# Optimization experiments

Measured on AMD Instinct MI355X. Metric: run time of the kernel, lower is better.

The kernel has to match this reference:

```python
import jax, jax.numpy as jnp
import numpy as np

N, E, G = 50000, 800000, 128
F_IN, H, NHID, C = 310, 128, 64, 2  # H = 2*nhid
NEG_SLOPE = 0.2


def setup_inputs() -> dict:
    key = jax.random.key(0)
    ks = jax.random.split(key, 16)
    def lin(k, fan_in, shape):
        return (jax.random.normal(k, shape, jnp.float32) / np.sqrt(fan_in)).astype(jnp.float32)
    return {
        "x": jax.random.normal(ks[0], (N, F_IN), jnp.float32),
        "edge_index": jax.random.randint(ks[1], (2, E), 0, N, dtype=jnp.int32),
        "batch": jnp.sort(jax.random.randint(ks[2], (N,), 0, G, dtype=jnp.int32)),
        "W1": lin(ks[3], F_IN, (F_IN, H)),
        "a_src1": lin(ks[4], H, (H,)),
        "a_dst1": lin(ks[5], H, (H,)),
        "b1": jnp.zeros((H,), jnp.float32),
        "W2": lin(ks[6], H, (H, H)),
        "a_src2": lin(ks[7], H, (H,)),
        "a_dst2": lin(ks[8], H, (H,)),
        "b2": jnp.zeros((H,), jnp.float32),
        "fc1_w": lin(ks[9], H, (H, NHID)),
        "fc1_b": jnp.zeros((NHID,), jnp.float32),
        "fc2_w": lin(ks[10], NHID, (NHID, C)),
        "fc2_b": jnp.zeros((C,), jnp.float32),
    }


def _gat(x, src, dst, W, a_src, a_dst, b):
    # PyG GATConv, heads=1: h = xW; e_ij = LeakyReLU(a_src.h_j + a_dst.h_i)
    h = x @ W                               # [N, H]
    asrc = h @ a_src                        # [N]
    adst = h @ a_dst                        # [N]
    e = jax.nn.leaky_relu(asrc[src] + adst[dst], NEG_SLOPE)  # [E']
    # segment softmax over incoming edges of each target node
    m = jax.ops.segment_max(e, dst, num_segments=N)
    ex = jnp.exp(e - m[dst])
    s = jax.ops.segment_sum(ex, dst, num_segments=N)
    w = ex / s[dst]                         # [E']
    out = jax.ops.segment_sum(h[src] * w[:, None], dst, num_segments=N)
    return out + b


def reference(x, edge_index, batch, W1, a_src1, a_dst1, b1,
              W2, a_src2, a_dst2, b2, fc1_w, fc1_b, fc2_w, fc2_b):
    # add self loops (GATConv default add_self_loops=True)
    ar = jnp.arange(N, dtype=edge_index.dtype)
    src = jnp.concatenate([edge_index[0], ar])
    dst = jnp.concatenate([edge_index[1], ar])

    h = jax.nn.selu(_gat(x, src, dst, W1, a_src1, a_dst1, b1))
    h = jax.nn.selu(_gat(h, src, dst, W2, a_src2, a_dst2, b2))

    # global mean pool over graphs
    summed = jax.ops.segment_sum(h, batch, num_segments=G)          # [G, H]
    cnt = jax.ops.segment_sum(jnp.ones((N,), h.dtype), batch, num_segments=G)
    pooled = jax.nn.selu(summed / jnp.maximum(cnt, 1.0)[:, None])

    z = jax.nn.selu(pooled @ fc1_w + fc1_b)  # dropout is identity in eval
    logits = z @ fc2_w + fc2_b
    return jax.nn.log_softmax(logits, axis=-1)
```

## Files before the change

### kernel.cpp

```cpp
#include <hip/hip_runtime.h>
#include <hip/hip_bf16.h>
#include <math.h>

#define NN 50000
#define NE 800000
#define NET (NE + NN)
#define FIN 310
#define HD 128
#define NHID 64
#define NCLS 2
#define NG 128
#define NEG_SLOPE 0.2f
#define KP1 320
#define KP2 128

#define SLOTS 64
#define NPART 8
#define PART_SZ (NN / NPART)
#define EPB 4096
#define NSLICE ((NET + EPB - 1) / EPB)
#define NSC (NSLICE * NPART)
#define GB1 ((NN + 63) / 64)
#define CASTW_GRID ((NE + 255) / 256)

#define SELU_SCALE 1.0507009873554804934193349852946f
#define SELU_ALPHA 1.6732632423543772848170429916717f

typedef short bf16x8 __attribute__((ext_vector_type(8)));
typedef float f32x4 __attribute__((ext_vector_type(4)));

__device__ __forceinline__ float selu(float x) {
    return SELU_SCALE * (x > 0.f ? x : SELU_ALPHA * (__expf(x) - 1.f));
}
__device__ __forceinline__ float lrelu(float x) {
    return x > 0.f ? x : NEG_SLOPE * x;
}
__device__ __forceinline__ unsigned short f2bf(float f) {
    unsigned int u = __float_as_uint(f);
    u = (u + 0x7fffu + ((u >> 16) & 1u)) >> 16;
    return (unsigned short)u;
}
__device__ __forceinline__ float bf2f(unsigned short b) {
    return __uint_as_float(((unsigned int)b) << 16);
}


__global__ void k_castW(const float* __restrict__ W1, const float* __restrict__ W2,
                        const int* __restrict__ ei,
                        unsigned short* __restrict__ W1p, unsigned short* __restrict__ W2p,
                        unsigned int* __restrict__ ep, int* __restrict__ cursor) {
    int i = blockIdx.x * blockDim.x + threadIdx.x;
    if (i < NN) cursor[i] = 0;
    const int N1 = HD * KP1;
    if (i < N1) {
        int n = i / KP1, k = i % KP1;
        unsigned short v = (k < FIN) ? f2bf(W1[(size_t)k * HD + n]) : (unsigned short)0;
        W1p[((k >> 3) * HD + n) * 8 + (k & 7)] = v;
    } else if (i - N1 < HD * KP2) {
        int j = i - N1;
        int n = j / KP2, k = j % KP2;
        W2p[((k >> 3) * HD + n) * 8 + (k & 7)] = f2bf(W2[(size_t)k * HD + n]);
    }
    if (i < NE)
        ep[i] = ((unsigned int)ei[i] << 16) | (unsigned int)ei[NE + i];
}


__device__ __forceinline__ void scatter_body(int slice, const unsigned int* __restrict__ ep,
                                             int* __restrict__ cursor,
                                             unsigned short* __restrict__ slots,
                                             int part) {
    int lo = part * PART_SZ;
    int base = slice * EPB + threadIdx.x;
#pragma unroll
    for (int k = 0; k < EPB / 256; ++k) {
        int i = base + k * 256;
        if (i >= NET) break;
        int d, s;
        if (i < NE) {
            unsigned int e = ep[i];
            d = (int)(e & 0xffffu);
            s = (int)(e >> 16);
        } else {
            d = i - NE; s = d;
        }
        if ((unsigned)(d - lo) < (unsigned)PART_SZ) {
            int pos = atomicAdd(&cursor[d], 1) & (SLOTS - 1);
            slots[(size_t)d * SLOTS + pos] = (unsigned short)s;
        }
    }
}


#define RGEMM_EPILOGUE                                                         \
    int gr_base = r0 + w * 16 + quad * 4;                                      \
    _Pragma("unroll")                                                          \
    for (int r = 0; r < 4; ++r) {                                              \
        int gr = gr_base + r;                                                  \
        if (gr < M) {                                                          \
            _Pragma("unroll")                                                  \
            for (int nt = 0; nt < 8; ++nt)                                     \
                C[(size_t)gr * HD + nt * 16 + l16] = f2bf(acc[nt][r]);         \
        }                                                                      \
    }                                                                          \
    _Pragma("unroll")                                                          \
    for (int r = 0; r < 4; ++r) {                                              \
        float s1 = 0.f, s2 = 0.f;                                              \
        _Pragma("unroll")                                                      \
        for (int nt = 0; nt < 8; ++nt) {                                       \
            int c = nt * 16 + l16;                                             \
            float v = acc[nt][r];                                              \
            s1 += v * a_src[c];                                                \
            s2 += v * a_dst[c];                                                \
        }                                                                      \
        _Pragma("unroll")                                                      \
        for (int off = 1; off < 16; off <<= 1) {                               \
            s1 += __shfl_xor(s1, off);                                         \
            s2 += __shfl_xor(s2, off);                                         \
        }                                                                      \
        int gr = gr_base + r;                                                  \
        if (l16 == 0 && gr < M) { asrcp[gr] = s1; adstp[gr] = s2; }            \
    }


__global__ __launch_bounds__(256) void k_pre(const float* __restrict__ A,
                                             const unsigned short* __restrict__ Bp,
                                             unsigned short* __restrict__ C,
                                             float* __restrict__ asrcp,
                                             float* __restrict__ adstp,
                                             const float* __restrict__ a_src,
                                             const float* __restrict__ a_dst,
                                             int M,
                                             const unsigned int* __restrict__ ep,
                                             int* __restrict__ cursor,
                                             unsigned short* __restrict__ slots) {
    if (blockIdx.x >= GB1) {
        int b = blockIdx.x - GB1;
        int part = (blockIdx.x + 2) & 7;
        scatter_body(b >> 3, ep, cursor, slots, part);
        return;
    }
    int t = threadIdx.x;
    int lane = t & 63, w = t >> 6;
    int quad = lane >> 4, l16 = lane & 15;
    int r0 = blockIdx.x * 64;

    int grow = r0 + w * 16 + l16;
    int arow = min(grow, M - 1);
    const float* ap = A + (size_t)arow * FIN + quad * 8;

    f32x4 acc[8] = {};

    float2 c0 = *(const float2*)(ap + 0);
    float2 c1 = *(const float2*)(ap + 2);
    float2 c2 = *(const float2*)(ap + 4);
    float2 c3 = *(const float2*)(ap + 6);
#pragma unroll
    for (int k0 = 0; k0 < 288; k0 += 32) {
        int kn = (k0 < 256) ? k0 + 32 : 256;
        float2 n0 = *(const float2*)(ap + kn + 0);
        float2 n1 = *(const float2*)(ap + kn + 2);
        float2 n2 = *(const float2*)(ap + kn + 4);
        float2 n3 = *(const float2*)(ap + kn + 6);
        union { bf16x8 v; unsigned short u[8]; } af;
        af.u[0] = f2bf(c0.x); af.u[1] = f2bf(c0.y);
        af.u[2] = f2bf(c1.x); af.u[3] = f2bf(c1.y);
        af.u[4] = f2bf(c2.x); af.u[5] = f2bf(c2.y);
        af.u[6] = f2bf(c3.x); af.u[7] = f2bf(c3.y);
        const unsigned short* bbase = Bp + ((size_t)(k0 >> 3) + quad) * (HD * 8) + l16 * 8;
#pragma unroll
        for (int nt = 0; nt < 8; ++nt) {
            bf16x8 bfr = *(const bf16x8*)(bbase + nt * 128);
            acc[nt] = __builtin_amdgcn_mfma_f32_16x16x32_bf16(af.v, bfr, acc[nt], 0, 0, 0);
        }
        c0 = n0; c1 = n1; c2 = n2; c3 = n3;
    }
    {
        int kb = 288 + quad * 8;
        const float* rp = A + (size_t)arow * FIN;
        union { bf16x8 v; unsigned short u[8]; } af;
#pragma unroll
        for (int j = 0; j < 8; ++j)
            af.u[j] = (kb + j < FIN) ? f2bf(rp[kb + j]) : (unsigned short)0;
        const unsigned short* bbase = Bp + ((size_t)(288 >> 3) + quad) * (HD * 8) + l16 * 8;
#pragma unroll
        for (int nt = 0; nt < 8; ++nt) {
            bf16x8 bfr = *(const bf16x8*)(bbase + nt * 128);
            acc[nt] = __builtin_amdgcn_mfma_f32_16x16x32_bf16(af.v, bfr, acc[nt], 0, 0, 0);
        }
    }
    RGEMM_EPILOGUE
}


__global__ __launch_bounds__(256) void k_gemm2(const unsigned short* __restrict__ A,
                                               const unsigned short* __restrict__ Bp,
                                               unsigned short* __restrict__ C,
                                               float* __restrict__ asrcp,
                                               float* __restrict__ adstp,
                                               const float* __restrict__ a_src,
                                               const float* __restrict__ a_dst,
                                               int M) {
    int t = threadIdx.x;
    int lane = t & 63, w = t >> 6;
    int quad = lane >> 4, l16 = lane & 15;
    int r0 = blockIdx.x * 64;

    int grow = r0 + w * 16 + l16;
    int arow = min(grow, M - 1);
    const unsigned short* aptr = A + (size_t)arow * KP2 + quad * 8;

    f32x4 acc[8] = {};
#pragma unroll
    for (int k0 = 0; k0 < KP2; k0 += 32) {
        bf16x8 af = *(const bf16x8*)(aptr + k0);
        const unsigned short* bbase = Bp + ((size_t)(k0 >> 3) + quad) * (HD * 8) + l16 * 8;
#pragma unroll
        for (int nt = 0; nt < 8; ++nt) {
            bf16x8 bfr = *(const bf16x8*)(bbase + nt * 128);
            acc[nt] = __builtin_amdgcn_mfma_f32_16x16x32_bf16(af, bfr, acc[nt], 0, 0, 0);
        }
    }
    RGEMM_EPILOGUE
}


__global__ __launch_bounds__(256) void k_gat(const unsigned short* __restrict__ h,
                                             const float* __restrict__ asrc,
                                             const float* __restrict__ adst,
                                             const int* __restrict__ degv,
                                             const unsigned short* __restrict__ slots,
                                             const float* __restrict__ bias,
                                             unsigned short* __restrict__ out) {
    int node = blockIdx.x * 4 + (threadIdx.x >> 6);
    int lane = threadIdx.x & 63;
    if (node >= NN) return;
    int g = lane >> 4, cl = lane & 15;
    int deg = degv[node];
    float adsti = adst[node];

    float2 acc2[4] = {};

    int cnt = min(deg, SLOTS);
    int s_c = 0; float p_c = 0.f;
    if (lane < cnt) {
        s_c = slots[(size_t)node * SLOTS + lane];
        p_c = __expf(lrelu(asrc[s_c] + adsti));
    }
    float den_l = p_c;
    int nt = (cnt + 3) >> 2;
    for (int t = 0; t < nt; t += 4) {
        float pv[4]; uint4 hv[4];
#pragma unroll
        for (int u = 0; u < 4; ++u) {
            int tt = t + u;
            bool valid = tt < nt;
            int e = (4 * tt + g) & 63;
            int s = __shfl(s_c, e);
            float p = __shfl(p_c, e);
            int sa = valid ? s : 0;
            pv[u] = valid ? p : 0.f;
            hv[u] = *(const uint4*)(h + (size_t)sa * HD + cl * 8);
        }
#pragma unroll
        for (int u = 0; u < 4; ++u) {
            float p = pv[u];
            unsigned int w0 = hv[u].x, w1 = hv[u].y, w2 = hv[u].z, w3 = hv[u].w;
            acc2[0].x += p * __uint_as_float(w0 << 16);
            acc2[0].y += p * __uint_as_float(w0 & 0xffff0000u);
            acc2[1].x += p * __uint_as_float(w1 << 16);
            acc2[1].y += p * __uint_as_float(w1 & 0xffff0000u);
            acc2[2].x += p * __uint_as_float(w2 << 16);
            acc2[2].y += p * __uint_as_float(w2 & 0xffff0000u);
            acc2[3].x += p * __uint_as_float(w3 << 16);
            acc2[3].y += p * __uint_as_float(w3 & 0xffff0000u);
        }
    }
#pragma unroll
    for (int k = 0; k < 4; ++k) {
        acc2[k].x += __shfl_xor(acc2[k].x, 16);
        acc2[k].y += __shfl_xor(acc2[k].y, 16);
        acc2[k].x += __shfl_xor(acc2[k].x, 32);
        acc2[k].y += __shfl_xor(acc2[k].y, 32);
    }
#pragma unroll
    for (int off = 32; off; off >>= 1)
        den_l += __shfl_xor(den_l, off);

    if (g == 0) {
        float inv = 1.f / den_l;
        int c0 = cl * 8;
        float4 b0 = *(const float4*)(bias + c0);
        float4 b1 = *(const float4*)(bias + c0 + 4);
        float v0 = selu(acc2[0].x * inv + b0.x);
        float v1 = selu(acc2[0].y * inv + b0.y);
        float v2 = selu(acc2[1].x * inv + b0.z);
        float v3 = selu(acc2[1].y * inv + b0.w);
        float v4 = selu(acc2[2].x * inv + b1.x);
        float v5 = selu(acc2[2].y * inv + b1.y);
        float v6 = selu(acc2[3].x * inv + b1.z);
        float v7 = selu(acc2[3].y * inv + b1.w);
        uint4 pk;
        pk.x = (unsigned int)f2bf(v0) | ((unsigned int)f2bf(v1) << 16);
        pk.y = (unsigned int)f2bf(v2) | ((unsigned int)f2bf(v3) << 16);
        pk.z = (unsigned int)f2bf(v4) | ((unsigned int)f2bf(v5) << 16);
        pk.w = (unsigned int)f2bf(v6) | ((unsigned int)f2bf(v7) << 16);
        *(uint4*)(out + (size_t)node * HD + c0) = pk;
    }
}


__device__ __forceinline__ int lower_bound_i(const int* a, int n, int key) {
    int lo = 0, hi = n;
    while (lo < hi) {
        int mid = (lo + hi) >> 1;
        if (a[mid] < key) lo = mid + 1; else hi = mid;
    }
    return lo;
}

__global__ __launch_bounds__(512) void k_poolfc(const unsigned short* __restrict__ x,
                                                const int* __restrict__ batch,
                                                const float* __restrict__ w1,
                                                const float* __restrict__ b1,
                                                const float* __restrict__ w2,
                                                const float* __restrict__ b2,
                                                float* __restrict__ out) {
    int g = blockIdx.x;
    int t = threadIdx.x;
    __shared__ int lo_s, hi_s;
    __shared__ float red[512];
    __shared__ float pooled_s[128];
    if (t == 0) {
        lo_s = lower_bound_i(batch, NN, g);
        hi_s = lower_bound_i(batch, NN, g + 1);
    }
    __syncthreads();
    int lo = lo_s, hi = hi_s;
    float acc = 0.f;
    for (int n = lo + (t >> 7); n < hi; n += 4)
        acc += bf2f(x[(size_t)n * HD + (t & 127)]);
    red[t] = acc;
    __syncthreads();
    if (t < 128) {
        float v = red[t] + red[t + 128] + red[t + 256] + red[t + 384];
        pooled_s[t] = selu(v / fmaxf((float)(hi - lo), 1.f));
    }
    __syncthreads();
    if (t < 64) {
        float z = 0.f;
#pragma unroll 8
        for (int k = 0; k < HD; ++k) z += pooled_s[k] * w1[k * NHID + t];
        z = selu(z + b1[t]);
        float p0 = z * w2[t * NCLS + 0];
        float p1 = z * w2[t * NCLS + 1];
        for (int off = 32; off; off >>= 1) {
            p0 += __shfl_down(p0, off);
            p1 += __shfl_down(p1, off);
        }
        if (t == 0) {
            float l0 = p0 + b2[0], l1 = p1 + b2[1];
            float m = fmaxf(l0, l1);
            float lse = m + __logf(__expf(l0 - m) + __expf(l1 - m));
            out[g * NCLS + 0] = l0 - lse;
            out[g * NCLS + 1] = l1 - lse;
        }
    }
}


static inline size_t align_up(size_t v, size_t a) { return (v + a - 1) / a * a; }

extern "C" void kernel_launch(void* const* d_in, const int* in_sizes, int n_in,
                              void* d_out, int out_size, void* d_ws, size_t ws_size,
                              hipStream_t stream) {
    const float* x      = (const float*)d_in[0];
    const int*   ei     = (const int*)d_in[1];
    const int*   batch  = (const int*)d_in[2];
    const float* W1     = (const float*)d_in[3];
    const float* a_src1 = (const float*)d_in[4];
    const float* a_dst1 = (const float*)d_in[5];
    const float* b1     = (const float*)d_in[6];
    const float* W2     = (const float*)d_in[7];
    const float* a_src2 = (const float*)d_in[8];
    const float* a_dst2 = (const float*)d_in[9];
    const float* b2     = (const float*)d_in[10];
    const float* fc1_w  = (const float*)d_in[11];
    const float* fc1_b  = (const float*)d_in[12];
    const float* fc2_w  = (const float*)d_in[13];
    const float* fc2_b  = (const float*)d_in[14];
    float* out = (float*)d_out;

    char* ws = (char*)d_ws;
    size_t off = 0;
    unsigned short* h1  = (unsigned short*)(ws + off); off = align_up(off + (size_t)NN * HD * 2, 256);
    unsigned short* o1  = (unsigned short*)(ws + off); off = align_up(off + (size_t)NN * HD * 2, 256);
    float* asrc = (float*)(ws + off); off = align_up(off + (size_t)NN * 4, 256);
    float* adst = (float*)(ws + off); off = align_up(off + (size_t)NN * 4, 256);
    int* cursor = (int*)(ws + off);   off = align_up(off + (size_t)NN * 4, 256);
    unsigned short* slots = (unsigned short*)(ws + off); off = align_up(off + (size_t)NN * SLOTS * 2, 256);
    unsigned short* W1p = (unsigned short*)(ws + off); off = align_up(off + (size_t)HD * KP1 * 2, 256);
    unsigned short* W2p = (unsigned short*)(ws + off); off = align_up(off + (size_t)HD * KP2 * 2, 256);
    unsigned int* epack = (unsigned int*)(ws + off); off = align_up(off + (size_t)NE * 4, 256);
    (void)ws_size;

    k_castW<<<CASTW_GRID, 256, 0, stream>>>(W1, W2, ei, W1p, W2p, epack, cursor);

    k_pre<<<GB1 + NSC, 256, 0, stream>>>(x, W1p, h1, asrc, adst, a_src1, a_dst1, NN,
                                         epack, cursor, slots);

    k_gat<<<(NN + 3) / 4, 256, 0, stream>>>(h1, asrc, adst, cursor, slots, b1, o1);

    k_gemm2<<<GB1, 256, 0, stream>>>(o1, W2p, h1, asrc, adst, a_src2, a_dst2, NN);
    k_gat<<<(NN + 3) / 4, 256, 0, stream>>>(h1, asrc, adst, cursor, slots, b2, o1);

    k_poolfc<<<NG, 512, 0, stream>>>(o1, batch, fc1_w, fc1_b, fc2_w, fc2_b, out);
}
```

Measured before the change: 291.1 us.

## Pre-bucket edges by destination partition before slot scatter

Result: slower. 324.7 us (+11.5%).

```diff
diff --git a/kernel.cpp b/kernel.cpp
--- a/kernel.cpp
+++ b/kernel.cpp
@@ -18,10 +18,11 @@
 #define NPART 8
 #define PART_SZ (NN / NPART)
 #define EPB 4096
-#define NSLICE ((NET + EPB - 1) / EPB)
-#define NSC (NSLICE * NPART)
+#define SL_P 27
+#define BCAP (SL_P * EPB)
+#define NSC (NPART * SL_P)
 #define GB1 ((NN + 63) / 64)
-#define CASTW_GRID ((NE + 255) / 256)
+#define CASTW_GRID ((NET + 255) / 256)
 
 #define SELU_SCALE 1.0507009873554804934193349852946f
 #define SELU_ALPHA 1.6732632423543772848170429916717f
@@ -48,7 +49,8 @@
 __global__ void k_castW(const float* __restrict__ W1, const float* __restrict__ W2,
                         const int* __restrict__ ei,
                         unsigned short* __restrict__ W1p, unsigned short* __restrict__ W2p,
-                        unsigned int* __restrict__ ep, int* __restrict__ cursor) {
+                        unsigned int* __restrict__ ebkt, int* __restrict__ bcnt,
+                        int* __restrict__ cursor) {
     int i = blockIdx.x * blockDim.x + threadIdx.x;
     if (i < NN) cursor[i] = 0;
     const int N1 = HD * KP1;
@@ -61,33 +63,46 @@
         int n = j / KP2, k = j % KP2;
         W2p[((k >> 3) * HD + n) * 8 + (k & 7)] = f2bf(W2[(size_t)k * HD + n]);
     }
-    if (i < NE)
-        ep[i] = ((unsigned int)ei[i] << 16) | (unsigned int)ei[NE + i];
-}
-
-
-__device__ __forceinline__ void scatter_body(int slice, const unsigned int* __restrict__ ep,
+
+    __shared__ int lcnt[NPART];
+    __shared__ int lbase[NPART];
+    if (threadIdx.x < NPART) lcnt[threadIdx.x] = 0;
+    __syncthreads();
+    int part = -1, lpos = 0; unsigned int pk = 0;
+    if (i < NET) {
+        int d, s;
+        if (i < NE) { s = ei[i]; d = ei[NE + i]; }
+        else        { d = i - NE; s = d; }
+        part = d / PART_SZ;
+        pk = ((unsigned int)s << 16) | (unsigned int)d;
+        lpos = atomicAdd(&lcnt[part], 1);
+    }
+    __syncthreads();
+    if (threadIdx.x < NPART)
+        lbase[threadIdx.x] = atomicAdd(&bcnt[threadIdx.x], lcnt[threadIdx.x]);
+    __syncthreads();
+    if (part >= 0)
+        ebkt[(size_t)part * BCAP + lbase[part] + lpos] = pk;
+}
+
+
+__device__ __forceinline__ void scatter_body(int slice, int part,
+                                             const unsigned int* __restrict__ ebkt,
+                                             const int* __restrict__ bcnt,
                                              int* __restrict__ cursor,
-                                             unsigned short* __restrict__ slots,
-                                             int part) {
-    int lo = part * PART_SZ;
+                                             unsigned short* __restrict__ slots) {
+    int n = bcnt[part];
+    const unsigned int* bp = ebkt + (size_t)part * BCAP;
     int base = slice * EPB + threadIdx.x;
 #pragma unroll
     for (int k = 0; k < EPB / 256; ++k) {
         int i = base + k * 256;
-        if (i >= NET) break;
-        int d, s;
-        if (i < NE) {
-            unsigned int e = ep[i];
-            d = (int)(e & 0xffffu);
-            s = (int)(e >> 16);
-        } else {
-            d = i - NE; s = d;
-        }
-        if ((unsigned)(d - lo) < (unsigned)PART_SZ) {
-            int pos = atomicAdd(&cursor[d], 1) & (SLOTS - 1);
-            slots[(size_t)d * SLOTS + pos] = (unsigned short)s;
-        }
+        if (i >= n) break;
+        unsigned int e = bp[i];
+        int d = (int)(e & 0xffffu);
+        int s = (int)(e >> 16);
+        int pos = atomicAdd(&cursor[d], 1) & (SLOTS - 1);
+        slots[(size_t)d * SLOTS + pos] = (unsigned short)s;
     }
 }
 
@@ -131,13 +146,13 @@
                                              const float* __restrict__ a_src,
                                              const float* __restrict__ a_dst,
                                              int M,
-                                             const unsigned int* __restrict__ ep,
+                                             const unsigned int* __restrict__ ebkt,
+                                             const int* __restrict__ bcnt,
                                              int* __restrict__ cursor,
                                              unsigned short* __restrict__ slots) {
     if (blockIdx.x >= GB1) {
         int b = blockIdx.x - GB1;
-        int part = (blockIdx.x + 2) & 7;
-        scatter_body(b >> 3, ep, cursor, slots, part);
+        scatter_body(b >> 3, b & (NPART - 1), ebkt, bcnt, cursor, slots);
         return;
     }
     int t = threadIdx.x;
@@ -401,13 +416,16 @@
     unsigned short* slots = (unsigned short*)(ws + off); off = align_up(off + (size_t)NN * SLOTS * 2, 256);
     unsigned short* W1p = (unsigned short*)(ws + off); off = align_up(off + (size_t)HD * KP1 * 2, 256);
     unsigned short* W2p = (unsigned short*)(ws + off); off = align_up(off + (size_t)HD * KP2 * 2, 256);
-    unsigned int* epack = (unsigned int*)(ws + off); off = align_up(off + (size_t)NE * 4, 256);
+    unsigned int* ebkt = (unsigned int*)(ws + off); off = align_up(off + (size_t)NPART * BCAP * 4, 256);
+    int* bcnt = (int*)(ws + off); off = align_up(off + (size_t)NPART * 4, 256);
     (void)ws_size;
 
-    k_castW<<<CASTW_GRID, 256, 0, stream>>>(W1, W2, ei, W1p, W2p, epack, cursor);
+    hipMemsetAsync(bcnt, 0, NPART * sizeof(int), stream);
+
+    k_castW<<<CASTW_GRID, 256, 0, stream>>>(W1, W2, ei, W1p, W2p, ebkt, bcnt, cursor);
 
     k_pre<<<GB1 + NSC, 256, 0, stream>>>(x, W1p, h1, asrc, adst, a_src1, a_dst1, NN,
-                                         epack, cursor, slots);
+                                         ebkt, bcnt, cursor, slots);
 
     k_gat<<<(NN + 3) / 4, 256, 0, stream>>>(h1, asrc, adst, cursor, slots, b1, o1);
 
```
